# Kernel tuning notes

Hardware: AMD Instinct MI355X
Metric: run time of the kernel (lower is better)

## Reference

```python
import jax, jax.numpy as jnp
import numpy as np
from jax import lax

B, S, D, E, H = 2, 2048, 1024, 8, 4096


def setup_inputs() -> dict:
    key = jax.random.key(0)
    ks = jax.random.split(key, 10)
    sc = 0.02  # GPT-style init scale
    return {
        "x": jax.random.normal(ks[0], (B, S, D), jnp.float32),
        "noise": jax.random.normal(ks[1], (B, S, E), jnp.float32),
        "w_route": jax.random.normal(ks[2], (D, E), jnp.float32) * sc,
        "b_route": jnp.zeros((E,), jnp.float32),
        "w_noise": jax.random.normal(ks[3], (D, E), jnp.float32) * sc,
        "b_noise": jnp.zeros((E,), jnp.float32),
        "w_fc": jax.random.normal(ks[4], (E, D, H), jnp.float32) * sc,
        "b_fc": jnp.zeros((E, H), jnp.float32),
        "w_proj": jax.random.normal(ks[5], (E, H, D), jnp.float32) * sc,
        "b_proj": jnp.zeros((E, D), jnp.float32),
        "top_k": 2,
    }


def reference(x, noise, w_route, b_route, w_noise, b_noise, w_fc, b_fc, w_proj, b_proj, top_k):
    # --- NoisyTopkRouter ---
    logits = x @ w_route + b_route                      # [B,S,E]
    noise_logits = x @ w_noise + b_noise                # [B,S,E]
    noisy = logits + noise * jax.nn.softplus(noise_logits)
    gate1 = jax.nn.softmax(noisy, axis=-1)              # dense gate (aux output)

    topk_vals, topk_idx = lax.top_k(noisy, top_k)       # [B,S,K]
    # softmax over sparse logits (-inf elsewhere) == softmax over the top-k values
    gk = jax.nn.softmax(topk_vals, axis=-1)             # [B,S,K]
    # scatter top-k gates back to the dense expert axis; non-selected experts get 0
    gating = (jax.nn.one_hot(topk_idx, E, dtype=x.dtype) * gk[..., None]).sum(-2)  # [B,S,E]

    # --- Experts (dense-over-experts, masked by gating; math identical to
    #     masked gather/scatter since non-selected gates are exactly 0) ---
    h = jnp.einsum('bsd,edh->bseh', x, w_fc) + b_fc     # [B,S,E,H]
    h = jax.nn.gelu(h, approximate=True)                # GELU(tanh)
    y = jnp.einsum('bseh,ehd->bsed', h, w_proj) + b_proj  # [B,S,E,D]
    out = jnp.einsum('bsed,bse->bsd', y, gating)        # weighted combine
    return out, gate1
```

## Files before the change

kernel.cpp:

```cpp
#include <hip/hip_runtime.h>
#include <cstdint>


#define DEV __device__ __forceinline__

typedef __attribute__((ext_vector_type(8))) short short8;
typedef __attribute__((ext_vector_type(4))) float floatx4;

constexpr int D_ = 1024, E_ = 8, H_ = 4096;
constexpr int NTOK = 4096;
constexpr int CAP  = 4096;
constexpr int TOTSLOT = NTOK * 2;

constexpr size_t O_COUNT = 0;
constexpr size_t O_OFFS  = 64;
constexpr size_t O_BTOK  = 128;
constexpr size_t O_BGATE = O_BTOK  + (size_t)E_ * CAP * 4;
constexpr size_t O_PAIR  = O_BGATE + (size_t)E_ * CAP * 4;
constexpr size_t O_XG    = (O_PAIR + (size_t)NTOK * 2 * 4 + 255) & ~(size_t)255;
constexpr size_t O_HBUF  = O_XG   + (size_t)TOTSLOT * D_ * 2;
constexpr size_t O_YBUF  = O_HBUF + (size_t)TOTSLOT * H_ * 2;
constexpr size_t O_WT    = O_YBUF + (size_t)TOTSLOT * D_ * 2;
constexpr size_t WS_NEED = O_WT   + (size_t)E_ * D_ * H_ * 2;

DEV float b2f(unsigned short u) {
    union { unsigned int i; float f; } v; v.i = ((unsigned int)u) << 16; return v.f;
}
DEV unsigned int f2b(float f) {
    union { float f; unsigned int i; } v; v.f = f;
    unsigned int r = v.i + 0x7fffu + ((v.i >> 16) & 1u);
    return (r >> 16) & 0xffffu;
}
DEV float gelu_tanh(float x) {
    float u = 0.7978845608028654f * (x + 0.044715f * x * x * x);
    u = fminf(fmaxf(u, -20.f), 20.f);
    float e = __expf(2.f * u);
    float t = (e - 1.f) / (e + 1.f);
    return 0.5f * x * (1.f + t);
}

typedef __attribute__((address_space(3))) unsigned int lds_u32_t;
typedef const __attribute__((address_space(1))) unsigned int g_u32_t;
DEV void gload16(const unsigned short* g, const unsigned short* l) {
    __builtin_amdgcn_global_load_lds((g_u32_t*)(size_t)g,
                                     (lds_u32_t*)(unsigned int)(size_t)l, 16, 0, 0);
}

__global__ __launch_bounds__(64) void zero_counts(int* counts) {
    if (threadIdx.x < E_) counts[threadIdx.x] = 0;
}

__global__ __launch_bounds__(256) void router_kernel(
    const float* __restrict__ x, const float* __restrict__ noise,
    const float* __restrict__ w_route, const float* __restrict__ b_route,
    const float* __restrict__ w_noise, const float* __restrict__ b_noise,
    float* __restrict__ out,
    int* counts, int* btok, float* bgate, int* pairs)
{
    int wave = threadIdx.x >> 6, lane = threadIdx.x & 63;
    int t = blockIdx.x * 4 + wave;

    double racc[E_], nacc[E_];
#pragma unroll
    for (int e = 0; e < E_; e++) { racc[e] = 0.0; nacc[e] = 0.0; }

#pragma unroll 4
    for (int i = 0; i < D_ / 64; i++) {
        int j = i * 64 + lane;
        float xv = x[(size_t)t * D_ + j];
        const float* wr = w_route + (size_t)j * E_;
        const float* wn = w_noise + (size_t)j * E_;
        float4 a0 = ((const float4*)wr)[0], a1 = ((const float4*)wr)[1];
        float4 c0 = ((const float4*)wn)[0], c1 = ((const float4*)wn)[1];
        const float rv[8] = {a0.x,a0.y,a0.z,a0.w,a1.x,a1.y,a1.z,a1.w};
        const float nv[8] = {c0.x,c0.y,c0.z,c0.w,c1.x,c1.y,c1.z,c1.w};
#pragma unroll
        for (int e = 0; e < E_; e++) {
            racc[e] += (double)(xv * rv[e]);
            nacc[e] += (double)(xv * nv[e]);
        }
    }
#pragma unroll
    for (int off = 32; off > 0; off >>= 1)
#pragma unroll
        for (int e = 0; e < E_; e++) {
            racc[e] += __shfl_down(racc[e], off);
            nacc[e] += __shfl_down(nacc[e], off);
        }

    if (lane == 0) {
        double nz[E_];
#pragma unroll
        for (int e = 0; e < E_; e++) {
            double lg = racc[e] + (double)b_route[e];
            double nl = nacc[e] + (double)b_noise[e];
            double sp = (nl > 0.0) ? nl + log1p(exp(-nl)) : log1p(exp(nl));
            nz[e] = lg + (double)noise[(size_t)t * E_ + e] * sp;
        }
        double mx = nz[0];
#pragma unroll
        for (int e = 1; e < E_; e++) mx = fmax(mx, nz[e]);
        double se = 0.0, ex[E_];
#pragma unroll
        for (int e = 0; e < E_; e++) { ex[e] = exp(nz[e] - mx); se += ex[e]; }
#pragma unroll
        for (int e = 0; e < E_; e++)
            out[(size_t)NTOK * D_ + (size_t)t * E_ + e] = (float)(ex[e] / se);
        double v0 = -1e300, v1 = -1e300; int i0 = 0, i1 = 0;
#pragma unroll
        for (int e = 0; e < E_; e++) {
            double v = nz[e];
            if (v > v0) { v1 = v0; i1 = i0; v0 = v; i0 = e; }
            else if (v > v1) { v1 = v; i1 = e; }
        }
        double g0 = 1.0 / (1.0 + exp(v1 - v0));
        float  g1 = (float)(1.0 - g0);
        int l0 = atomicAdd(&counts[i0], 1);
        int l1 = atomicAdd(&counts[i1], 1);
        btok[i0 * CAP + l0] = t;  bgate[i0 * CAP + l0] = (float)g0;
        btok[i1 * CAP + l1] = t;  bgate[i1 * CAP + l1] = g1;
        pairs[2 * t]     = (i0 << 16) | l0;
        pairs[2 * t + 1] = (i1 << 16) | l1;
    }
}

__global__ __launch_bounds__(64) void offsets_kernel(const int* counts, int* offs) {
    if (threadIdx.x == 0) {
        int a = 0;
        for (int e = 0; e < E_; e++) { offs[e] = a; a += counts[e]; }
        offs[E_] = a;
    }
}

__global__ __launch_bounds__(256) void gather_x(
    const float* __restrict__ x, const int* __restrict__ pairs,
    const int* __restrict__ offs, unsigned short* __restrict__ xg)
{
    int t = blockIdx.x;
    int c = threadIdx.x * 4;
    float4 v = *(const float4*)(x + (size_t)t * D_ + c);
    uint2 o;
    o.x = f2b(v.x) | (f2b(v.y) << 16);
    o.y = f2b(v.z) | (f2b(v.w) << 16);
    int p0 = pairs[2 * t], p1 = pairs[2 * t + 1];
    size_t r0 = (size_t)(offs[p0 >> 16] + (p0 & 0xffff)) * D_;
    size_t r1 = (size_t)(offs[p1 >> 16] + (p1 & 0xffff)) * D_;
    *(uint2*)(xg + r0 + c) = o;
    *(uint2*)(xg + r1 + c) = o;
}

__global__ __launch_bounds__(256) void transpose_w(
    const float* __restrict__ w, unsigned short* __restrict__ wT, int K, int N)
{
    __shared__ unsigned short t[64][65];
    const int e  = blockIdx.z;
    const int k0 = blockIdx.y * 64;
    const int n0 = blockIdx.x * 64;
    const int r  = threadIdx.x >> 2;
    const int c4 = (threadIdx.x & 3) * 16;
    const float* src = w + ((size_t)e * K + k0 + r) * N + n0 + c4;
#pragma unroll
    for (int i = 0; i < 4; i++) {
        float4 v = ((const float4*)src)[i];
        t[r][c4 + 4*i + 0] = (unsigned short)f2b(v.x);
        t[r][c4 + 4*i + 1] = (unsigned short)f2b(v.y);
        t[r][c4 + 4*i + 2] = (unsigned short)f2b(v.z);
        t[r][c4 + 4*i + 3] = (unsigned short)f2b(v.w);
    }
    __syncthreads();
    unsigned short* dstp = wT + ((size_t)e * N + n0 + r) * K + k0 + c4;
    unsigned short tmp[16];
#pragma unroll
    for (int i = 0; i < 16; i++) tmp[i] = t[c4 + i][r];
#pragma unroll
    for (int h = 0; h < 2; h++) {
        uint4 pk;
        pk.x = (unsigned int)tmp[8*h+0] | ((unsigned int)tmp[8*h+1] << 16);
        pk.y = (unsigned int)tmp[8*h+2] | ((unsigned int)tmp[8*h+3] << 16);
        pk.z = (unsigned int)tmp[8*h+4] | ((unsigned int)tmp[8*h+5] << 16);
        pk.w = (unsigned int)tmp[8*h+6] | ((unsigned int)tmp[8*h+7] << 16);
        ((uint4*)dstp)[h] = pk;
    }
}

template <int KD, int ND, bool FC>
__global__ __launch_bounds__(256) void moe_gemm3(
    const unsigned short* __restrict__ A,
    const unsigned short* __restrict__ wT,
    const float* __restrict__ bias32,
    unsigned short* __restrict__ dst,
    const int* __restrict__ counts, const int* __restrict__ offs,
    const float* __restrict__ bgate)
{
    const int lin = blockIdx.x;
    const int xcd = lin & 7, slot = lin >> 3;
    int e, mt, nt;
    if (FC) {
        nt = xcd * 4 + (slot & 3);
        mt = (slot >> 2) & 31;
        e  = slot >> 7;
    } else {
        nt = xcd;
        mt = slot & 31;
        e  = slot >> 5;
    }
    const int cnt = counts[e];
    const int m0 = mt * 128;
    if (m0 >= cnt) return;
    const int n0 = nt * 128;
    const int off = offs[e];

    __shared__ unsigned short As[128 * 64];
    __shared__ unsigned short Bs[128 * 64];

    const int tid = threadIdx.x;
    const int waveid = tid >> 6, lane = tid & 63;
    const int sr = lane >> 3;
    const int g  = lane & 7;
    const int scol = ((g ^ sr) * 8);

    const unsigned short* aAddr[4];
    const unsigned short* bAddr[4];
#pragma unroll
    for (int c = 0; c < 4; c++) {
        int ar = m0 + (waveid * 4 + c) * 8 + sr;
        if (ar > cnt - 1) ar = cnt - 1;
        aAddr[c] = A + (size_t)(off + ar) * KD + scol;
        int br = n0 + (waveid * 4 + c) * 8 + sr;
        bAddr[c] = wT + ((size_t)e * ND + br) * KD + scol;
    }
    const int ldsChunk = (waveid * 4) * 512;

    const int wm = (waveid & 1) * 64, wn = (waveid >> 1) * 64;
    const int lrow = lane & 15, quad = lane >> 4;

    floatx4 acc[4][4];
#pragma unroll
    for (int fm = 0; fm < 4; fm++)
#pragma unroll
        for (int fn = 0; fn < 4; fn++) acc[fm][fn] = (floatx4)0.f;

    for (int k0 = 0; k0 < KD; k0 += 64) {
        __syncthreads();
#pragma unroll
        for (int c = 0; c < 4; c++) {
            gload16(aAddr[c] + k0, &As[ldsChunk + c * 512]);
            gload16(bAddr[c] + k0, &Bs[ldsChunk + c * 512]);
        }
        __syncthreads();
#pragma unroll
        for (int ks = 0; ks < 2; ks++) {
            short8 af[4], bfr[4];
#pragma unroll
            for (int f = 0; f < 4; f++) {
                int Ra = wm + f * 16 + lrow;
                int Rb = wn + f * 16 + lrow;
                af[f]  = *(const short8*)&As[Ra * 64 + ((ks * 4 + quad) ^ (Ra & 7)) * 8];
                bfr[f] = *(const short8*)&Bs[Rb * 64 + ((ks * 4 + quad) ^ (Rb & 7)) * 8];
            }
#pragma unroll
            for (int fm = 0; fm < 4; fm++)
#pragma unroll
                for (int fn = 0; fn < 4; fn++)
                    acc[fm][fn] = __builtin_amdgcn_mfma_f32_16x16x32_bf16(
                        af[fm], bfr[fn], acc[fm][fn], 0, 0, 0);
        }
    }

    const int gc = n0 + wn + lrow;
    float bcol[4];
#pragma unroll
    for (int fn = 0; fn < 4; fn++) bcol[fn] = bias32[(size_t)e * ND + gc + fn * 16];

#pragma unroll
    for (int fm = 0; fm < 4; fm++) {
        int srow0 = m0 + wm + fm * 16 + quad * 4;
#pragma unroll
        for (int r = 0; r < 4; r++) {
            int srow = srow0 + r;
            if (srow < cnt) {
                size_t base = (size_t)(off + srow) * ND;
                if (FC) {
#pragma unroll
                    for (int fn = 0; fn < 4; fn++) {
                        float v = acc[fm][fn][r] + bcol[fn];
                        dst[base + gc + fn * 16] = (unsigned short)f2b(gelu_tanh(v));
                    }
                } else {
                    float gt = bgate[e * CAP + srow];
#pragma unroll
                    for (int fn = 0; fn < 4; fn++) {
                        float v = (acc[fm][fn][r] + bcol[fn]) * gt;
                        dst[base + gc + fn * 16] = (unsigned short)f2b(v);
                    }
                }
            }
        }
    }
}

__global__ __launch_bounds__(256) void combine_kernel(
    const unsigned short* __restrict__ ybuf, const int* __restrict__ pairs,
    const int* __restrict__ offs, float* __restrict__ out)
{
    int t = blockIdx.x;
    int p0 = pairs[2 * t], p1 = pairs[2 * t + 1];
    size_t r0 = (size_t)(offs[p0 >> 16] + (p0 & 0xffff)) * D_;
    size_t r1 = (size_t)(offs[p1 >> 16] + (p1 & 0xffff)) * D_;
    int c = threadIdx.x * 4;
    uint2 a = *(const uint2*)(ybuf + r0 + c);
    uint2 b = *(const uint2*)(ybuf + r1 + c);
    float4 o;
    o.x = b2f((unsigned short)(a.x & 0xffffu)) + b2f((unsigned short)(b.x & 0xffffu));
    o.y = b2f((unsigned short)(a.x >> 16))     + b2f((unsigned short)(b.x >> 16));
    o.z = b2f((unsigned short)(a.y & 0xffffu)) + b2f((unsigned short)(b.y & 0xffffu));
    o.w = b2f((unsigned short)(a.y >> 16))     + b2f((unsigned short)(b.y >> 16));
    *(float4*)(out + (size_t)t * D_ + c) = o;
}

extern "C" void kernel_launch(void* const* d_in, const int* in_sizes, int n_in,
                              void* d_out, int out_size, void* d_ws, size_t ws_size,
                              hipStream_t stream) {
    if (ws_size < WS_NEED) return;

    const float* x       = (const float*)d_in[0];
    const float* noise   = (const float*)d_in[1];
    const float* w_route = (const float*)d_in[2];
    const float* b_route = (const float*)d_in[3];
    const float* w_noise = (const float*)d_in[4];
    const float* b_noise = (const float*)d_in[5];
    const float* w_fc    = (const float*)d_in[6];
    const float* b_fc    = (const float*)d_in[7];
    const float* w_proj  = (const float*)d_in[8];
    const float* b_proj  = (const float*)d_in[9];

    char* ws = (char*)d_ws;
    int*   counts = (int*)(ws + O_COUNT);
    int*   offs   = (int*)(ws + O_OFFS);
    int*   btok   = (int*)(ws + O_BTOK);
    float* bgate  = (float*)(ws + O_BGATE);
    int*   pairs  = (int*)(ws + O_PAIR);
    unsigned short* xg   = (unsigned short*)(ws + O_XG);
    unsigned short* hbuf = (unsigned short*)(ws + O_HBUF);
    unsigned short* ybuf = (unsigned short*)(ws + O_YBUF);
    unsigned short* wT   = (unsigned short*)(ws + O_WT);

    zero_counts<<<dim3(1), dim3(64), 0, stream>>>(counts);
    router_kernel<<<dim3(NTOK / 4), dim3(256), 0, stream>>>(
        x, noise, w_route, b_route, w_noise, b_noise, (float*)d_out,
        counts, btok, bgate, pairs);
    offsets_kernel<<<dim3(1), dim3(64), 0, stream>>>(counts, offs);
    gather_x<<<dim3(NTOK), dim3(256), 0, stream>>>(x, pairs, offs, xg);

    transpose_w<<<dim3(H_ / 64, D_ / 64, E_), dim3(256), 0, stream>>>(w_fc, wT, D_, H_);
    moe_gemm3<D_, H_, true><<<dim3(8 * 32 * 32), dim3(256), 0, stream>>>(
        xg, wT, b_fc, hbuf, counts, offs, bgate);

    transpose_w<<<dim3(D_ / 64, H_ / 64, E_), dim3(256), 0, stream>>>(w_proj, wT, H_, D_);
    moe_gemm3<H_, D_, false><<<dim3(8 * 32 * 8), dim3(256), 0, stream>>>(
        hbuf, wT, b_proj, ybuf, counts, offs, bgate);

    combine_kernel<<<dim3(NTOK), dim3(256), 0, stream>>>(ybuf, pairs, offs, (float*)d_out);
}
```

Baseline: 716.1 us.

## Add four-stage LDS ring buffer with async prefetch to MoE GEMM

```diff
diff --git a/kernel.cpp b/kernel.cpp
--- a/kernel.cpp
+++ b/kernel.cpp
@@ -210,8 +210,9 @@
     const int n0 = nt * 128;
     const int off = offs[e];
 
-    __shared__ unsigned short As[128 * 64];
-    __shared__ unsigned short Bs[128 * 64];
+    extern __shared__ unsigned short smem[];
+    constexpr int SEG  = 2 * 128 * 64;
+    constexpr int BOFF = 128 * 64;
 
     const int tid = threadIdx.x;
     const int waveid = tid >> 6, lane = tid & 63;
@@ -240,14 +241,33 @@
 #pragma unroll
         for (int fn = 0; fn < 4; fn++) acc[fm][fn] = (floatx4)0.f;
 
-    for (int k0 = 0; k0 < KD; k0 += 64) {
-        __syncthreads();
+    const int nk = KD / 64;
+
+#pragma unroll
+    for (int p = 0; p < 3; p++) {
+        unsigned short* buf = smem + p * SEG;
+        const int k0 = p * 64;
 #pragma unroll
         for (int c = 0; c < 4; c++) {
-            gload16(aAddr[c] + k0, &As[ldsChunk + c * 512]);
-            gload16(bAddr[c] + k0, &Bs[ldsChunk + c * 512]);
-        }
-        __syncthreads();
+            gload16(aAddr[c] + k0, &buf[ldsChunk + c * 512]);
+            gload16(bAddr[c] + k0, &buf[BOFF + ldsChunk + c * 512]);
+        }
+    }
+    asm volatile("s_waitcnt vmcnt(16)" ::: "memory");
+    __builtin_amdgcn_s_barrier();
+
+    for (int t = 0; t < nk - 3; ++t) {
+        {
+            unsigned short* buf = smem + ((t + 3) & 3) * SEG;
+            const int k0 = (t + 3) * 64;
+#pragma unroll
+            for (int c = 0; c < 4; c++) {
+                gload16(aAddr[c] + k0, &buf[ldsChunk + c * 512]);
+                gload16(bAddr[c] + k0, &buf[BOFF + ldsChunk + c * 512]);
+            }
+        }
+        const unsigned short* As = smem + (t & 3) * SEG;
+        const unsigned short* Bs = As + BOFF;
 #pragma unroll
         for (int ks = 0; ks < 2; ks++) {
             short8 af[4], bfr[4];
@@ -265,6 +285,31 @@
                     acc[fm][fn] = __builtin_amdgcn_mfma_f32_16x16x32_bf16(
                         af[fm], bfr[fn], acc[fm][fn], 0, 0, 0);
         }
+        asm volatile("s_waitcnt vmcnt(16)" ::: "memory");
+        __builtin_amdgcn_s_barrier();
+    }
+
+    for (int t = nk - 3; t < nk; ++t) {
+        const unsigned short* As = smem + (t & 3) * SEG;
+        const unsigned short* Bs = As + BOFF;
+#pragma unroll
+        for (int ks = 0; ks < 2; ks++) {
+            short8 af[4], bfr[4];
+#pragma unroll
+            for (int f = 0; f < 4; f++) {
+                int Ra = wm + f * 16 + lrow;
+                int Rb = wn + f * 16 + lrow;
+                af[f]  = *(const short8*)&As[Ra * 64 + ((ks * 4 + quad) ^ (Ra & 7)) * 8];
+                bfr[f] = *(const short8*)&Bs[Rb * 64 + ((ks * 4 + quad) ^ (Rb & 7)) * 8];
+            }
+#pragma unroll
+            for (int fm = 0; fm < 4; fm++)
+#pragma unroll
+                for (int fn = 0; fn < 4; fn++)
+                    acc[fm][fn] = __builtin_amdgcn_mfma_f32_16x16x32_bf16(
+                        af[fm], bfr[fn], acc[fm][fn], 0, 0, 0);
+        }
+        __syncthreads();
     }
 
     const int gc = n0 + wn + lrow;
@@ -345,6 +390,8 @@
     unsigned short* ybuf = (unsigned short*)(ws + O_YBUF);
     unsigned short* wT   = (unsigned short*)(ws + O_WT);
 
+    constexpr unsigned GEMM_LDS = 4u * 2u * 128u * 64u * 2u;
+
     zero_counts<<<dim3(1), dim3(64), 0, stream>>>(counts);
     router_kernel<<<dim3(NTOK / 4), dim3(256), 0, stream>>>(
         x, noise, w_route, b_route, w_noise, b_noise, (float*)d_out,
@@ -353,11 +400,11 @@
     gather_x<<<dim3(NTOK), dim3(256), 0, stream>>>(x, pairs, offs, xg);
 
     transpose_w<<<dim3(H_ / 64, D_ / 64, E_), dim3(256), 0, stream>>>(w_fc, wT, D_, H_);
-    moe_gemm3<D_, H_, true><<<dim3(8 * 32 * 32), dim3(256), 0, stream>>>(
+    moe_gemm3<D_, H_, true><<<dim3(8 * 32 * 32), dim3(256), GEMM_LDS, stream>>>(
         xg, wT, b_fc, hbuf, counts, offs, bgate);
 
     transpose_w<<<dim3(D_ / 64, H_ / 64, E_), dim3(256), 0, stream>>>(w_proj, wT, H_, D_);
-    moe_gemm3<H_, D_, false><<<dim3(8 * 32 * 8), dim3(256), 0, stream>>>(
+    moe_gemm3<H_, D_, false><<<dim3(8 * 32 * 8), dim3(256), GEMM_LDS, stream>>>(
         hbuf, wT, b_proj, ybuf, counts, offs, bgate);
 
     combine_kernel<<<dim3(NTOK), dim3(256), 0, stream>>>(ybuf, pairs, offs, (float*)d_out);
```

After: 728.3 us. About the same (+1.7%).
